# Optimization experiments

Hardware: AMD Instinct MI355X
Metric: run time of the kernel (lower is better)

Reference implementation:

```python
import jax, jax.numpy as jnp
import numpy as np

E = 400000   # total edges
G = 64       # num graphs
H = 256      # hidden_dim
NN = 20000   # node id range
FRONTIER_BONUS = 0.5


def layer_norm(x, g, b, eps=1e-5):
    m = jnp.mean(x, axis=-1, keepdims=True)
    v = jnp.var(x, axis=-1, keepdims=True)
    return (x - m) / jnp.sqrt(v + eps) * g + b


def setup_inputs() -> dict:
    key = jax.random.key(0)
    ks = jax.random.split(key, 20)
    s = 0.02
    inp = {
        "edge_tokens": jax.random.normal(ks[0], (E, H), jnp.float32),
        "question_tokens": jax.random.normal(ks[1], (G, H), jnp.float32),
        "edge_batch": jnp.sort(jax.random.randint(ks[2], (E,), 0, G)),
        "selected_mask": jax.random.bernoulli(ks[3], 0.3, (E,)),
        "edge_heads": jax.random.randint(ks[4], (E,), 0, NN),
        "edge_tails": jax.random.randint(ks[5], (E,), 0, NN),
        "current_tail": jax.random.randint(ks[6], (G,), 0, NN),
        # edge_proj params: LayerNorm(H+2) -> Linear(H+2,H) -> GELU -> Linear(H,H) -> GELU
        "ln1_g": jnp.ones((H + 2,), jnp.float32),
        "ln1_b": jnp.zeros((H + 2,), jnp.float32),
        "W1": s * jax.random.normal(ks[7], (H + 2, H), jnp.float32),
        "b1": jnp.zeros((H,), jnp.float32),
        "W2": s * jax.random.normal(ks[8], (H, H), jnp.float32),
        "b2": jnp.zeros((H,), jnp.float32),
        # selection_head: Linear(H,1)
        "sel_w": s * jax.random.normal(ks[9], (H, 1), jnp.float32),
        "sel_b": jnp.zeros((1,), jnp.float32),
        # stop_head: LayerNorm(2H) -> Linear(2H,H) -> GELU -> Linear(H,1)
        "ln2_g": jnp.ones((2 * H,), jnp.float32),
        "ln2_b": jnp.zeros((2 * H,), jnp.float32),
        "sW1": s * jax.random.normal(ks[10], (2 * H, H), jnp.float32),
        "sb1": jnp.zeros((H,), jnp.float32),
        "sW2": s * jax.random.normal(ks[11], (H, 1), jnp.float32),
        "sb2": jnp.zeros((1,), jnp.float32),
    }
    return inp


def reference(edge_tokens, question_tokens, edge_batch, selected_mask,
              edge_heads, edge_tails, current_tail,
              ln1_g, ln1_b, W1, b1, W2, b2, sel_w, sel_b,
              ln2_g, ln2_b, sW1, sb1, sW2, sb2):
    num_graphs = question_tokens.shape[0]
    candidate = ~selected_mask
    cur_e = current_tail[edge_batch]                       # [E] gather by graph id
    frontier = candidate & ((edge_heads == cur_e) | (edge_tails == cur_e))
    aux = jnp.stack([candidate.astype(jnp.float32), frontier.astype(jnp.float32)], axis=-1)
    x = jnp.concatenate([edge_tokens, aux], axis=-1)       # [E, H+2]
    h = layer_norm(x, ln1_g, ln1_b)
    h = jax.nn.gelu(h @ W1 + b1, approximate=False)        # Dropout is identity in eval
    h = jax.nn.gelu(h @ W2 + b2, approximate=False)        # edge_repr [E, H]
    edge_logits = (h @ sel_w)[:, 0] + sel_b[0]
    edge_logits = edge_logits + FRONTIER_BONUS * frontier.astype(jnp.float32)
    counts = jax.ops.segment_sum(jnp.ones((h.shape[0],), jnp.float32), edge_batch, num_segments=num_graphs)
    counts = jnp.clip(counts, 1.0)                          # bincount.clamp(min=1)
    pooled = jax.ops.segment_sum(h, edge_batch, num_segments=num_graphs) / counts[:, None]
    s_in = jnp.concatenate([pooled, question_tokens], axis=-1)  # [G, 2H]
    s = layer_norm(s_in, ln2_g, ln2_b)
    s = jax.nn.gelu(s @ sW1 + sb1, approximate=False)
    stop_logits = (s @ sW2)[:, 0] + sb2[0]
    return edge_logits, stop_logits, pooled
```

## Files before the change

### kernel.cpp

```cpp
#include <hip/hip_runtime.h>
#include <hip/hip_bf16.h>
#include <cstdint>


typedef __bf16 bf16x8 __attribute__((ext_vector_type(8)));
typedef float  f32x4  __attribute__((ext_vector_type(4)));

__device__ __forceinline__ float gelu_f(float x) {
  float x2 = x * x;
  float t1 = __builtin_fmaf(0.1029444f, x2, 2.3022078f);
  float a  = x * t1;
  float e;
  asm("v_exp_f32 %0, %1" : "=v"(e) : "v"(a));
  float r;
  asm("v_rcp_f32 %0, %1" : "=v"(r) : "v"(e + 1.0f));
  return x - x * r;
}

__device__ __forceinline__ bf16x8 as_frag(uint4 u) {
  union { uint4 u; bf16x8 f; } c; c.u = u; return c.f;
}

__global__ void prep_pack(const float* __restrict__ W1, const float* __restrict__ W2,
                          const float* __restrict__ ln1g,
                          __bf16* __restrict__ W1p, __bf16* __restrict__ W2p) {
  int gid = blockIdx.x * blockDim.x + threadIdx.x;
  int m  = gid >> 13;
  int b  = (gid >> 6) & 127;
  int l  = gid & 63;
  int kt = b >> 4, nt = b & 15;
  int k0 = kt * 32 + ((l >> 4) << 3);
  int n  = nt * 16 + (l & 15);
  const float* W = m ? W2 : W1;
  bf16x8 v;
#pragma unroll
  for (int i = 0; i < 8; ++i) {
    int k = k0 + i;
    float wv = W[k * 256 + n];
    if (!m) wv *= ln1g[k];
    v[i] = (__bf16)wv;
  }
  __bf16* dst = m ? W2p : W1p;
  *(bf16x8*)(dst + (size_t)(b * 64 + l) * 8) = v;
}

__global__ void prep_vec(const float* __restrict__ W1, const float* __restrict__ ln1g,
                         const float* __restrict__ ln1b, const float* __restrict__ b1,
                         const unsigned* __restrict__ smask_words,
                         float* __restrict__ C0, float* __restrict__ GW6,
                         float* __restrict__ GW7, int* __restrict__ maskIsByte) {
  __shared__ float red[4][256];
  const int n = threadIdx.x & 255, c = threadIdx.x >> 8;
  const int k0 = c * 64, k1 = (c == 3) ? 258 : k0 + 64;
  float s = 0.f;
#pragma unroll 4
  for (int k = k0; k < k1; ++k) s += ln1b[k] * W1[k * 256 + n];
  red[c][n] = s;
  __syncthreads();
  if (c == 0) {
    C0[n]  = b1[n] + red[0][n] + red[1][n] + red[2][n] + red[3][n];
    GW6[n] = ln1g[256] * W1[256 * 256 + n];
    GW7[n] = ln1g[257] * W1[257 * 256 + n];
  }
  if (threadIdx.x == 0) {
    int big = 0;
    for (int i = 0; i < 64; ++i) { if (smask_words[i] > 1u) big = 1; }
    *maskIsByte = big;
  }
}

#define EPB 64

__device__ __forceinline__ void gemm8_pre(const char* __restrict__ Wp,
                                          const char* aBase, unsigned swA,
                                          unsigned gA, int bOff,
                                          uint4 (&bv)[4], f32x4 (&acc)[4][4]) {
#pragma unroll
  for (int kt = 0; kt < 8; ++kt) {
    uint4 bn[4];
    if (kt < 7) {
#pragma unroll
      for (int cf = 0; cf < 4; ++cf)
        bn[cf] = *(const uint4*)(Wp + (kt + 1) * 16384 + bOff + (cf << 10));
    }
    bf16x8 av[4];
#pragma unroll
    for (int rf = 0; rf < 4; ++rf)
      av[rf] = *(const bf16x8*)(aBase + rf * 8192 + (((unsigned)(kt * 64) + gA) ^ swA));
#pragma unroll
    for (int rf = 0; rf < 4; ++rf)
#pragma unroll
      for (int cf = 0; cf < 4; ++cf)
        acc[rf][cf] = __builtin_amdgcn_mfma_f32_16x16x32_bf16(av[rf], as_frag(bv[cf]),
                                                              acc[rf][cf], 0, 0, 0);
#pragma unroll
    for (int cf = 0; cf < 4; ++cf) bv[cf] = bn[cf];
  }
}

__global__ __launch_bounds__(256, 3) void edge_kernel(
    const float* __restrict__ tok, const int* __restrict__ ebatch,
    const unsigned char* __restrict__ smaskB,
    const int* __restrict__ eheads, const int* __restrict__ etails,
    const int* __restrict__ curtail,
    const __bf16* __restrict__ W1p, const __bf16* __restrict__ W2p,
    const float* __restrict__ C0v, const float* __restrict__ GW6v,
    const float* __restrict__ GW7v, const float* __restrict__ b2v,
    const float* __restrict__ selwv, const float* __restrict__ selbv,
    const int* __restrict__ maskFlag,
    float* __restrict__ outLogits, float* __restrict__ pooledAcc,
    float* __restrict__ cnts) {
  __shared__ __align__(16) char As_[64 * 512];
  __shared__ float sZa0[64], sZa1[64], sFront[64];
  __shared__ float sLog[64][4];
  __shared__ int sG[64];

  const int t = threadIdx.x;
  const int w = t >> 6, l = t & 63;
  const int base = blockIdx.x * EPB;
  const int bOff = (w << 12) + (l << 4);
  const int mb = *maskFlag;

  uint4 wb0[4];
#pragma unroll
  for (int cf = 0; cf < 4; ++cf)
    wb0[cf] = *(const uint4*)((const char*)W1p + bOff + (cf << 10));

  const int e = t >> 2, q = t & 3;
  const int ge = base + e;
  {
    const float* rp = tok + (size_t)ge * 256 + q * 4;
    float s = 0.f, s2 = 0.f;
#pragma unroll
    for (int j = 0; j < 16; ++j) {
      float4 v = *(const float4*)(rp + j * 16);
      s  += v.x + v.y + v.z + v.w;
      s2 += v.x * v.x + v.y * v.y + v.z * v.z + v.w * v.w;
    }
    float candf = 0.f, frontf = 0.f;
    if (q == 0) {
      int g  = ebatch[ge];
      int mv = mb ? (int)smaskB[ge] : ((const int*)smaskB)[ge];
      int cand = (mv == 0);
      int cur  = curtail[g];
      int fr   = cand && ((eheads[ge] == cur) || (etails[ge] == cur));
      candf = (float)cand; frontf = (float)fr;
      sFront[e] = (float)fr; sG[e] = g;
    }
    const float a0 = __shfl(candf,  l & 60);
    const float a1 = __shfl(frontf, l & 60);
    s  += __shfl_xor(s, 1);  s  += __shfl_xor(s, 2);
    s2 += __shfl_xor(s2, 1); s2 += __shfl_xor(s2, 2);
    s += a0 + a1; s2 += a0 + a1;
    const float mean = s * (1.0f / 258.0f);
    const float var  = s2 * (1.0f / 258.0f) - mean * mean;
    const float rstd = rsqrtf(var + 1e-5f);
    const float nm   = -mean * rstd;
    const unsigned sw = (unsigned)(e & 7) << 4;
    const float* rp2 = rp;
    asm volatile("" : "+v"(rp2));
#pragma unroll
    for (int j = 0; j < 16; ++j) {
      float4 v = *(const float4*)(rp2 + j * 16);
      union { __bf16 h[4]; uint2 u; } cv;
      cv.h[0] = (__bf16)__builtin_fmaf(v.x, rstd, nm);
      cv.h[1] = (__bf16)__builtin_fmaf(v.y, rstd, nm);
      cv.h[2] = (__bf16)__builtin_fmaf(v.z, rstd, nm);
      cv.h[3] = (__bf16)__builtin_fmaf(v.w, rstd, nm);
      unsigned off = (unsigned)(q * 8 + j * 32);
      *(uint2*)(As_ + e * 512 + (off ^ sw)) = cv.u;
    }
    if (q == 0) {
      sZa0[e] = __builtin_fmaf(a0, rstd, nm);
      sZa1[e] = __builtin_fmaf(a1, rstd, nm);
    }
  }
  __syncthreads();

  if (t == 0) {
    int cg = sG[0]; float run = 1.f;
    for (int ee = 1; ee < EPB; ++ee) {
      int g = sG[ee];
      if (g == cg) run += 1.f;
      else { atomicAdd(&cnts[cg], run); cg = g; run = 1.f; }
    }
    atomicAdd(&cnts[cg], run);
  }

  const int rA = l & 15;
  const int r0 = (l >> 4) << 2;
  f32x4 acc[4][4];
  {
    float c0r[4], w6r[4], w7r[4];
#pragma unroll
    for (int cf = 0; cf < 4; ++cf) {
      int col = w * 64 + cf * 16 + rA;
      c0r[cf] = C0v[col]; w6r[cf] = GW6v[col]; w7r[cf] = GW7v[col];
    }
    f32x4 za0q[4], za1q[4];
#pragma unroll
    for (int rf = 0; rf < 4; ++rf) {
      za0q[rf] = *(const f32x4*)&sZa0[rf * 16 + r0];
      za1q[rf] = *(const f32x4*)&sZa1[rf * 16 + r0];
    }
#pragma unroll
    for (int rf = 0; rf < 4; ++rf)
#pragma unroll
      for (int cf = 0; cf < 4; ++cf)
#pragma unroll
        for (int i = 0; i < 4; ++i)
          acc[rf][cf][i] = c0r[cf] + za0q[rf][i] * w6r[cf] + za1q[rf][i] * w7r[cf];
  }

  const unsigned swA = (unsigned)(rA & 7) << 4;
  const unsigned gA  = (unsigned)((l >> 4) << 4);
  const char* aBase  = As_ + rA * 512;

  gemm8_pre((const char*)W1p, aBase, swA, gA, bOff, wb0, acc);
  __syncthreads();

#pragma unroll
  for (int cf = 0; cf < 4; ++cf)
    wb0[cf] = *(const uint4*)((const char*)W2p + bOff + (cf << 10));

#pragma unroll
  for (int rf = 0; rf < 4; ++rf)
#pragma unroll
    for (int i = 0; i < 4; ++i) {
      int row = rf * 16 + r0 + i;
      char* rowp = As_ + row * 512;
      unsigned sw = (unsigned)(row & 7) << 4;
#pragma unroll
      for (int cf = 0; cf < 4; ++cf) {
        int col = w * 64 + cf * 16 + rA;
        *(__bf16*)(rowp + (((unsigned)(col * 2)) ^ sw)) = (__bf16)gelu_f(acc[rf][cf][i]);
      }
    }
  __syncthreads();

#pragma unroll
  for (int cf = 0; cf < 4; ++cf) {
    float bb = b2v[w * 64 + cf * 16 + rA];
#pragma unroll
    for (int rf = 0; rf < 4; ++rf)
#pragma unroll
      for (int i = 0; i < 4; ++i) acc[rf][cf][i] = bb;
  }
  gemm8_pre((const char*)W2p, aBase, swA, gA, bOff, wb0, acc);

#pragma unroll
  for (int rf = 0; rf < 4; ++rf)
#pragma unroll
    for (int cf = 0; cf < 4; ++cf)
#pragma unroll
      for (int i = 0; i < 4; ++i) acc[rf][cf][i] = gelu_f(acc[rf][cf][i]);

  {
    float lwr[4];
#pragma unroll
    for (int cf = 0; cf < 4; ++cf) lwr[cf] = selwv[w * 64 + cf * 16 + rA];
#pragma unroll
    for (int rf = 0; rf < 4; ++rf)
#pragma unroll
      for (int i = 0; i < 4; ++i) {
        float p = acc[rf][0][i] * lwr[0] + acc[rf][1][i] * lwr[1]
                + acc[rf][2][i] * lwr[2] + acc[rf][3][i] * lwr[3];
        p += __shfl_xor(p, 1); p += __shfl_xor(p, 2);
        p += __shfl_xor(p, 4); p += __shfl_xor(p, 8);
        if (rA == 0) sLog[rf * 16 + r0 + i][w] = p;
      }
  }
  __syncthreads();
  if (t < 64)
    outLogits[base + t] = sLog[t][0] + sLog[t][1] + sLog[t][2] + sLog[t][3]
                        + selbv[0] + 0.5f * sFront[t];

  if (sG[0] == sG[EPB - 1]) {
    int g = sG[0];
#pragma unroll
    for (int cf = 0; cf < 4; ++cf) {
      float sv = 0.f;
#pragma unroll
      for (int rf = 0; rf < 4; ++rf)
#pragma unroll
        for (int i = 0; i < 4; ++i) sv += acc[rf][cf][i];
      sv += __shfl_xor(sv, 16);
      sv += __shfl_xor(sv, 32);
      if (l < 16) atomicAdd(&pooledAcc[g * 256 + w * 64 + cf * 16 + l], sv);
    }
  } else {
#pragma unroll
    for (int rf = 0; rf < 4; ++rf)
#pragma unroll
      for (int i = 0; i < 4; ++i) {
        int row = rf * 16 + r0 + i;
        int g = sG[row];
#pragma unroll
        for (int cf = 0; cf < 4; ++cf)
          atomicAdd(&pooledAcc[g * 256 + w * 64 + cf * 16 + rA], acc[rf][cf][i]);
      }
  }
}

__global__ __launch_bounds__(256) void stop_kernel(
    const float* __restrict__ pooledAcc, const float* __restrict__ cnts,
    const float* __restrict__ qtok,
    const float* __restrict__ ln2g, const float* __restrict__ ln2b,
    const float* __restrict__ sW1, const float* __restrict__ sb1,
    const float* __restrict__ sW2, const float* __restrict__ sb2,
    float* __restrict__ outStop, float* __restrict__ outPooled) {
  __shared__ float sIn[512], sLn[512], sRed[8];
  const int t = threadIdx.x, g = blockIdx.x;
  const int w = t >> 6, l = t & 63;
  float c = fmaxf(cnts[g], 1.0f);
  float p = pooledAcc[g * 256 + t] / c;
  outPooled[g * 256 + t] = p;
  sIn[t] = p;
  sIn[256 + t] = qtok[g * 256 + t];
  __syncthreads();
  float a = sIn[t], b = sIn[256 + t];
  float s = a + b, s2 = a * a + b * b;
#pragma unroll
  for (int m = 1; m < 64; m <<= 1) { s += __shfl_xor(s, m); s2 += __shfl_xor(s2, m); }
  if (l == 0) { sRed[w] = s; sRed[4 + w] = s2; }
  __syncthreads();
  s  = sRed[0] + sRed[1] + sRed[2] + sRed[3];
  s2 = sRed[4] + sRed[5] + sRed[6] + sRed[7];
  const float mean = s * (1.0f / 512.0f);
  const float var  = s2 * (1.0f / 512.0f) - mean * mean;
  const float rstd = rsqrtf(var + 1e-5f);
  sLn[t]       = (a - mean) * rstd * ln2g[t] + ln2b[t];
  sLn[256 + t] = (b - mean) * rstd * ln2g[256 + t] + ln2b[256 + t];
  __syncthreads();
  float accv = sb1[t];
#pragma unroll 8
  for (int k = 0; k < 512; ++k) accv += sLn[k] * sW1[k * 256 + t];
  float u = gelu_f(accv);
  float part = u * sW2[t];
#pragma unroll
  for (int m = 1; m < 64; m <<= 1) part += __shfl_xor(part, m);
  if (l == 0) sRed[w] = part;
  __syncthreads();
  if (t == 0) outStop[g] = sRed[0] + sRed[1] + sRed[2] + sRed[3] + sb2[0];
}

extern "C" void kernel_launch(void* const* d_in, const int* in_sizes, int n_in,
                              void* d_out, int out_size, void* d_ws, size_t ws_size,
                              hipStream_t stream) {
  const float* tok   = (const float*)d_in[0];
  const float* qtok  = (const float*)d_in[1];
  const int* ebatch  = (const int*)d_in[2];
  const void* smask  = d_in[3];
  const int* eheads  = (const int*)d_in[4];
  const int* etails  = (const int*)d_in[5];
  const int* curtail = (const int*)d_in[6];
  const float* ln1g  = (const float*)d_in[7];
  const float* ln1b  = (const float*)d_in[8];
  const float* W1    = (const float*)d_in[9];
  const float* b1    = (const float*)d_in[10];
  const float* W2    = (const float*)d_in[11];
  const float* b2    = (const float*)d_in[12];
  const float* selw  = (const float*)d_in[13];
  const float* selb  = (const float*)d_in[14];
  const float* ln2g  = (const float*)d_in[15];
  const float* ln2b  = (const float*)d_in[16];
  const float* sW1   = (const float*)d_in[17];
  const float* sb1   = (const float*)d_in[18];
  const float* sW2   = (const float*)d_in[19];
  const float* sb2   = (const float*)d_in[20];

  const int E = in_sizes[2];
  const int G = in_sizes[1] / 256;

  char* ws = (char*)d_ws;
  __bf16* W1p   = (__bf16*)(ws);
  __bf16* W2p   = (__bf16*)(ws + 131072);
  float*  C0    = (float*)(ws + 262144);
  float*  GW6   = (float*)(ws + 263168);
  float*  GW7   = (float*)(ws + 264192);
  float*  pooled= (float*)(ws + 265216);
  float*  cnts  = (float*)(ws + 330752);
  int*    mflag = (int*)(ws + 331008);
  (void)ws_size; (void)n_in; (void)out_size;

  hipMemsetAsync(ws + 265216, 0, 65536 + 256, stream);

  prep_pack<<<64, 256, 0, stream>>>(W1, W2, ln1g, W1p, W2p);
  prep_vec<<<1, 1024, 0, stream>>>(W1, ln1g, ln1b, b1, (const unsigned*)smask,
                                   C0, GW6, GW7, mflag);
  edge_kernel<<<E / EPB, 256, 0, stream>>>(
      tok, ebatch, (const unsigned char*)smask, eheads, etails, curtail,
      W1p, W2p, C0, GW6, GW7, b2, selw, selb, mflag,
      (float*)d_out, pooled, cnts);
  stop_kernel<<<G, 256, 0, stream>>>(pooled, cnts, qtok, ln2g, ln2b,
                                     sW1, sb1, sW2, sb2,
                                     (float*)d_out + E, (float*)d_out + E + G);
}
```

Before: 311.5 us.

## Split edge tile across eight waves in a 2x4 row/column grid

Doubles the edge kernel block from 256 to 512 threads. Each wave now computes 32 rows by 64 columns instead of 64 by 64, halving the accumulator count per thread, and the LayerNorm prologue uses 8 threads per edge. The goal is lower register pressure, higher occupancy and more waves to hide memory latency. The cost is that each W1/W2 fragment is loaded by twice as many waves per block, and barriers now span more waves.

```diff
diff --git a/kernel.cpp b/kernel.cpp
--- a/kernel.cpp
+++ b/kernel.cpp
@@ -74,7 +74,7 @@
 __device__ __forceinline__ void gemm8_pre(const char* __restrict__ Wp,
                                           const char* aBase, unsigned swA,
                                           unsigned gA, int bOff,
-                                          uint4 (&bv)[4], f32x4 (&acc)[4][4]) {
+                                          uint4 (&bv)[4], f32x4 (&acc)[2][4]) {
 #pragma unroll
   for (int kt = 0; kt < 8; ++kt) {
     uint4 bn[4];
@@ -83,12 +83,12 @@
       for (int cf = 0; cf < 4; ++cf)
         bn[cf] = *(const uint4*)(Wp + (kt + 1) * 16384 + bOff + (cf << 10));
     }
-    bf16x8 av[4];
-#pragma unroll
-    for (int rf = 0; rf < 4; ++rf)
+    bf16x8 av[2];
+#pragma unroll
+    for (int rf = 0; rf < 2; ++rf)
       av[rf] = *(const bf16x8*)(aBase + rf * 8192 + (((unsigned)(kt * 64) + gA) ^ swA));
 #pragma unroll
-    for (int rf = 0; rf < 4; ++rf)
+    for (int rf = 0; rf < 2; ++rf)
 #pragma unroll
       for (int cf = 0; cf < 4; ++cf)
         acc[rf][cf] = __builtin_amdgcn_mfma_f32_16x16x32_bf16(av[rf], as_frag(bv[cf]),
@@ -98,7 +98,7 @@
   }
 }
 
-__global__ __launch_bounds__(256, 3) void edge_kernel(
+__global__ __launch_bounds__(512, 4) void edge_kernel(
     const float* __restrict__ tok, const int* __restrict__ ebatch,
     const unsigned char* __restrict__ smaskB,
     const int* __restrict__ eheads, const int* __restrict__ etails,
@@ -117,8 +117,9 @@
 
   const int t = threadIdx.x;
   const int w = t >> 6, l = t & 63;
+  const int wr = w >> 2, wc = w & 3;
   const int base = blockIdx.x * EPB;
-  const int bOff = (w << 12) + (l << 4);
+  const int bOff = (wc << 12) + (l << 4);
   const int mb = *maskFlag;
 
   uint4 wb0[4];
@@ -126,14 +127,14 @@
   for (int cf = 0; cf < 4; ++cf)
     wb0[cf] = *(const uint4*)((const char*)W1p + bOff + (cf << 10));
 
-  const int e = t >> 2, q = t & 3;
+  const int e = t >> 3, q = t & 7;
   const int ge = base + e;
   {
     const float* rp = tok + (size_t)ge * 256 + q * 4;
     float s = 0.f, s2 = 0.f;
 #pragma unroll
-    for (int j = 0; j < 16; ++j) {
-      float4 v = *(const float4*)(rp + j * 16);
+    for (int j = 0; j < 8; ++j) {
+      float4 v = *(const float4*)(rp + j * 32);
       s  += v.x + v.y + v.z + v.w;
       s2 += v.x * v.x + v.y * v.y + v.z * v.z + v.w * v.w;
     }
@@ -147,10 +148,10 @@
       candf = (float)cand; frontf = (float)fr;
       sFront[e] = (float)fr; sG[e] = g;
     }
-    const float a0 = __shfl(candf,  l & 60);
-    const float a1 = __shfl(frontf, l & 60);
-    s  += __shfl_xor(s, 1);  s  += __shfl_xor(s, 2);
-    s2 += __shfl_xor(s2, 1); s2 += __shfl_xor(s2, 2);
+    const float a0 = __shfl(candf,  l & 56);
+    const float a1 = __shfl(frontf, l & 56);
+    s  += __shfl_xor(s, 1);  s  += __shfl_xor(s, 2);  s  += __shfl_xor(s, 4);
+    s2 += __shfl_xor(s2, 1); s2 += __shfl_xor(s2, 2); s2 += __shfl_xor(s2, 4);
     s += a0 + a1; s2 += a0 + a1;
     const float mean = s * (1.0f / 258.0f);
     const float var  = s2 * (1.0f / 258.0f) - mean * mean;
@@ -160,14 +161,14 @@
     const float* rp2 = rp;
     asm volatile("" : "+v"(rp2));
 #pragma unroll
-    for (int j = 0; j < 16; ++j) {
-      float4 v = *(const float4*)(rp2 + j * 16);
+    for (int j = 0; j < 8; ++j) {
+      float4 v = *(const float4*)(rp2 + j * 32);
       union { __bf16 h[4]; uint2 u; } cv;
       cv.h[0] = (__bf16)__builtin_fmaf(v.x, rstd, nm);
       cv.h[1] = (__bf16)__builtin_fmaf(v.y, rstd, nm);
       cv.h[2] = (__bf16)__builtin_fmaf(v.z, rstd, nm);
       cv.h[3] = (__bf16)__builtin_fmaf(v.w, rstd, nm);
-      unsigned off = (unsigned)(q * 8 + j * 32);
+      unsigned off = (unsigned)(q * 8 + j * 64);
       *(uint2*)(As_ + e * 512 + (off ^ sw)) = cv.u;
     }
     if (q == 0) {
@@ -189,22 +190,22 @@
 
   const int rA = l & 15;
   const int r0 = (l >> 4) << 2;
-  f32x4 acc[4][4];
+  f32x4 acc[2][4];
   {
     float c0r[4], w6r[4], w7r[4];
 #pragma unroll
     for (int cf = 0; cf < 4; ++cf) {
-      int col = w * 64 + cf * 16 + rA;
+      int col = wc * 64 + cf * 16 + rA;
       c0r[cf] = C0v[col]; w6r[cf] = GW6v[col]; w7r[cf] = GW7v[col];
     }
-    f32x4 za0q[4], za1q[4];
-#pragma unroll
-    for (int rf = 0; rf < 4; ++rf) {
-      za0q[rf] = *(const f32x4*)&sZa0[rf * 16 + r0];
-      za1q[rf] = *(const f32x4*)&sZa1[rf * 16 + r0];
-    }
-#pragma unroll
-    for (int rf = 0; rf < 4; ++rf)
+    f32x4 za0q[2], za1q[2];
+#pragma unroll
+    for (int rf = 0; rf < 2; ++rf) {
+      za0q[rf] = *(const f32x4*)&sZa0[wr * 32 + rf * 16 + r0];
+      za1q[rf] = *(const f32x4*)&sZa1[wr * 32 + rf * 16 + r0];
+    }
+#pragma unroll
+    for (int rf = 0; rf < 2; ++rf)
 #pragma unroll
       for (int cf = 0; cf < 4; ++cf)
 #pragma unroll
@@ -214,7 +215,7 @@
 
   const unsigned swA = (unsigned)(rA & 7) << 4;
   const unsigned gA  = (unsigned)((l >> 4) << 4);
-  const char* aBase  = As_ + rA * 512;
+  const char* aBase  = As_ + (wr * 32 + rA) * 512;
 
   gemm8_pre((const char*)W1p, aBase, swA, gA, bOff, wb0, acc);
   __syncthreads();
@@ -224,15 +225,15 @@
     wb0[cf] = *(const uint4*)((const char*)W2p + bOff + (cf << 10));
 
 #pragma unroll
-  for (int rf = 0; rf < 4; ++rf)
+  for (int rf = 0; rf < 2; ++rf)
 #pragma unroll
     for (int i = 0; i < 4; ++i) {
-      int row = rf * 16 + r0 + i;
+      int row = wr * 32 + rf * 16 + r0 + i;
       char* rowp = As_ + row * 512;
       unsigned sw = (unsigned)(row & 7) << 4;
 #pragma unroll
       for (int cf = 0; cf < 4; ++cf) {
-        int col = w * 64 + cf * 16 + rA;
+        int col = wc * 64 + cf * 16 + rA;
         *(__bf16*)(rowp + (((unsigned)(col * 2)) ^ sw)) = (__bf16)gelu_f(acc[rf][cf][i]);
       }
     }
@@ -240,16 +241,16 @@
 
 #pragma unroll
   for (int cf = 0; cf < 4; ++cf) {
-    float bb = b2v[w * 64 + cf * 16 + rA];
-#pragma unroll
-    for (int rf = 0; rf < 4; ++rf)
+    float bb = b2v[wc * 64 + cf * 16 + rA];
+#pragma unroll
+    for (int rf = 0; rf < 2; ++rf)
 #pragma unroll
       for (int i = 0; i < 4; ++i) acc[rf][cf][i] = bb;
   }
   gemm8_pre((const char*)W2p, aBase, swA, gA, bOff, wb0, acc);
 
 #pragma unroll
-  for (int rf = 0; rf < 4; ++rf)
+  for (int rf = 0; rf < 2; ++rf)
 #pragma unroll
     for (int cf = 0; cf < 4; ++cf)
 #pragma unroll
@@ -258,16 +259,16 @@
   {
     float lwr[4];
 #pragma unroll
-    for (int cf = 0; cf < 4; ++cf) lwr[cf] = selwv[w * 64 + cf * 16 + rA];
-#pragma unroll
-    for (int rf = 0; rf < 4; ++rf)
+    for (int cf = 0; cf < 4; ++cf) lwr[cf] = selwv[wc * 64 + cf * 16 + rA];
+#pragma unroll
+    for (int rf = 0; rf < 2; ++rf)
 #pragma unroll
       for (int i = 0; i < 4; ++i) {
         float p = acc[rf][0][i] * lwr[0] + acc[rf][1][i] * lwr[1]
                 + acc[rf][2][i] * lwr[2] + acc[rf][3][i] * lwr[3];
         p += __shfl_xor(p, 1); p += __shfl_xor(p, 2);
         p += __shfl_xor(p, 4); p += __shfl_xor(p, 8);
-        if (rA == 0) sLog[rf * 16 + r0 + i][w] = p;
+        if (rA == 0) sLog[wr * 32 + rf * 16 + r0 + i][wc] = p;
       }
   }
   __syncthreads();
@@ -281,23 +282,23 @@
     for (int cf = 0; cf < 4; ++cf) {
       float sv = 0.f;
 #pragma unroll
-      for (int rf = 0; rf < 4; ++rf)
+      for (int rf = 0; rf < 2; ++rf)
 #pragma unroll
         for (int i = 0; i < 4; ++i) sv += acc[rf][cf][i];
       sv += __shfl_xor(sv, 16);
       sv += __shfl_xor(sv, 32);
-      if (l < 16) atomicAdd(&pooledAcc[g * 256 + w * 64 + cf * 16 + l], sv);
+      if (l < 16) atomicAdd(&pooledAcc[g * 256 + wc * 64 + cf * 16 + l], sv);
     }
   } else {
 #pragma unroll
-    for (int rf = 0; rf < 4; ++rf)
+    for (int rf = 0; rf < 2; ++rf)
 #pragma unroll
       for (int i = 0; i < 4; ++i) {
-        int row = rf * 16 + r0 + i;
+        int row = wr * 32 + rf * 16 + r0 + i;
         int g = sG[row];
 #pragma unroll
         for (int cf = 0; cf < 4; ++cf)
-          atomicAdd(&pooledAcc[g * 256 + w * 64 + cf * 16 + rA], acc[rf][cf][i]);
+          atomicAdd(&pooledAcc[g * 256 + wc * 64 + cf * 16 + rA], acc[rf][cf][i]);
       }
   }
 }
@@ -388,7 +389,7 @@
   prep_pack<<<64, 256, 0, stream>>>(W1, W2, ln1g, W1p, W2p);
   prep_vec<<<1, 1024, 0, stream>>>(W1, ln1g, ln1b, b1, (const unsigned*)smask,
                                    C0, GW6, GW7, mflag);
-  edge_kernel<<<E / EPB, 256, 0, stream>>>(
+  edge_kernel<<<E / EPB, 512, 0, stream>>>(
       tok, ebatch, (const unsigned char*)smask, eheads, etails, curtail,
       W1p, W2p, C0, GW6, GW7, b2, selw, selb, mflag,
       (float*)d_out, pooled, cnts);
```

New measurement: 336.9 us. 1.08x slower.
